# Performance work log

Hardware: AMD Instinct MI355X
Metric: run time of the kernel (lower is better)

## Reference

```python
import jax, jax.numpy as jnp
import numpy as np

EPS = 1e-5
NB, NP, NA, NROT = 16, 1024, 12, 60
C0, C1 = 64, 128
CIN, CFEAT, COUT = 256, 512, 256


def _bn(x, g, b):
    # training-mode BatchNorm1d: stats over batch (+ spatial) dims, channel dim 1
    axes = (0,) if x.ndim == 2 else (0, 2)
    m = x.mean(axis=axes, keepdims=True)
    v = x.var(axis=axes, keepdims=True)
    sh = [1] * x.ndim; sh[1] = -1
    return (x - m) * jax.lax.rsqrt(v + EPS) * g.reshape(sh) + b.reshape(sh)


def _hat(v):  # (n,3) -> (n,3,3) skew-symmetric
    z = jnp.zeros_like(v[:, 0])
    return jnp.stack([z, -v[:, 2], v[:, 1],
                      v[:, 2], z, -v[:, 0],
                      -v[:, 1], v[:, 0], z], axis=-1).reshape(-1, 3, 3)


def _exp_so3(v):  # Rodrigues formula, (n,3) -> (n,3,3)
    theta = jnp.linalg.norm(v, axis=-1, keepdims=True)  # (n,1)
    k = v / jnp.where(theta < 1e-8, 1.0, theta)
    K = _hat(k)
    s = jnp.sin(theta)[..., None]
    c = (1.0 - jnp.cos(theta))[..., None]
    I = jnp.eye(3, dtype=v.dtype)
    return I + s * K + c * (K @ K)


def _pointnet(xyz, feats, W, b, g, bb):
    # PointnetSO3Conv: concat xyz (expanded over anchors) with feats, 1x1 conv, max over points
    nb, _, npts, na = feats.shape
    x = jnp.concatenate([jnp.broadcast_to(xyz[:, :, :, None], (nb, 3, npts, na)), feats], axis=1)
    y = jnp.einsum('oc,bcpa->bopa', W, x) + b[None, :, None, None]
    y = y.max(axis=2)  # max over points -> (nb, o, na)
    return jax.nn.relu(_bn(y, g, bb))


def setup_inputs() -> dict:
    key = jax.random.key(0)
    ks = iter(jax.random.split(key, 64))
    def nrm(shape, s=0.1):
        return jax.random.normal(next(ks), shape, dtype=jnp.float32) * s
    d = {
        'xyz0': nrm((NB, 3, NP), 1.0),
        'feats0': nrm((NB, C0, NP, NA), 1.0),
        'xyz1': nrm((NB, 3, NP), 1.0),
        'feats1': nrm((NB, C1, NP, NA), 1.0),
        'trace_idx': jax.random.randint(next(ks), (NA, NROT), 0, NA),
        'anchors': nrm((NROT, 3, 3), 1.0),
        'pn0_W': nrm((C0, C0 + 3)), 'pn0_b': nrm((C0,)), 'pn0_g': jnp.ones((C0,), jnp.float32), 'pn0_bb': jnp.zeros((C0,), jnp.float32),
        'pn1_W': nrm((C1, C1 + 3)), 'pn1_b': nrm((C1,)), 'pn1_g': jnp.ones((C1,), jnp.float32), 'pn1_bb': jnp.zeros((C1,), jnp.float32),
        'lin_W': nrm((CIN, C0 + C1)), 'lin_b': nrm((CIN,)), 'lin_g': jnp.ones((CIN,), jnp.float32), 'lin_bb': jnp.zeros((CIN,), jnp.float32),
        'feat_W': nrm((CFEAT, CIN * NA)), 'feat_b': nrm((CFEAT,)), 'feat_g': jnp.ones((CFEAT,), jnp.float32), 'feat_bb': jnp.zeros((CFEAT,), jnp.float32),
        'att_W1': nrm((128, CFEAT)), 'att_b1': nrm((128,)), 'att_g': jnp.ones((128,), jnp.float32), 'att_bb': jnp.zeros((128,), jnp.float32),
        'att_W2': nrm((1, 128)), 'att_b2': nrm((1,)),
        'reg_W1': nrm((128, CFEAT)), 'reg_b1': nrm((128,)), 'reg_g': jnp.ones((128,), jnp.float32), 'reg_bb': jnp.zeros((128,), jnp.float32),
        'reg_W2': nrm((7, 128)), 'reg_b2': nrm((7,)),
        'out_W1': nrm((CFEAT, CFEAT)), 'out_b1': nrm((CFEAT,)), 'out_g': jnp.ones((CFEAT,), jnp.float32), 'out_bb': jnp.zeros((CFEAT,), jnp.float32),
        'out_W2': nrm((COUT, CFEAT)), 'out_b2': nrm((COUT,)),
    }
    return d


def reference(xyz0, feats0, xyz1, feats1, trace_idx, anchors,
              pn0_W, pn0_b, pn0_g, pn0_bb, pn1_W, pn1_b, pn1_g, pn1_bb,
              lin_W, lin_b, lin_g, lin_bb, feat_W, feat_b, feat_g, feat_bb,
              att_W1, att_b1, att_g, att_bb, att_W2, att_b2,
              reg_W1, reg_b1, reg_g, reg_bb, reg_W2, reg_b2,
              out_W1, out_b1, out_g, out_bb, out_W2, out_b2):
    nb = feats0.shape[0]
    # _pooling: per-level pointnet + BN + relu, concat, pn_linear + pn_bn
    p0 = _pointnet(xyz0, feats0, pn0_W, pn0_b, pn0_g, pn0_bb)
    p1 = _pointnet(xyz1, feats1, pn1_W, pn1_b, pn1_g, pn1_bb)
    x = jnp.concatenate([p0, p1], axis=1)                                   # (nb, 192, na)
    x = _bn(jnp.einsum('oc,bca->boa', lin_W, x) + lin_b[None, :, None], lin_g, lin_bb)  # (nb,256,na)
    # gather trace_idx_ori and flatten channel x anchor dims
    x = x[:, :, trace_idx].reshape(nb, CIN * NA, NROT)                      # (nb,3072,60)
    xf = jax.nn.relu(_bn(jnp.einsum('oc,bca->boa', feat_W, x) + feat_b[None, :, None], feat_g, feat_bb))  # (nb,512,60)
    h = jax.nn.relu(_bn(jnp.einsum('oc,bca->boa', reg_W1, xf) + reg_b1[None, :, None], reg_g, reg_bb))
    residual = (jnp.einsum('oc,bca->boa', reg_W2, h) + reg_b2[None, :, None]).transpose(0, 2, 1)  # (nb,60,7)
    res_D = residual[:, :, :3] / jnp.linalg.norm(residual[:, :, :3], axis=-1, keepdims=True)
    res_N = (jax.nn.sigmoid(residual[:, :, 3]) - 0.5) * jnp.pi / 5
    res_V = res_D * res_N[..., None]
    res_R = _exp_so3(res_V.reshape(-1, 3)).reshape(nb, NROT, 3, 3)
    res_T = residual[:, :, 4:]
    pred_R = jnp.einsum('tij,btjk->btik', anchors, res_R)
    # attention head + softmax over 60 rotations
    a = jax.nn.relu(_bn(jnp.einsum('oc,bca->boa', att_W1, xf) + att_b1[None, :, None], att_g, att_bb))
    logits = (jnp.einsum('oc,bca->boa', att_W2, a) + att_b2[None, :, None])[:, 0]   # (nb,60)
    x_attn = jax.nn.softmax(logits, axis=-1)
    # max-pool over rotations + out MLP
    xm = xf.max(axis=-1)                                                    # (nb,512)
    o = jax.nn.relu(_bn(xm @ out_W1.T + out_b1, out_g, out_bb))
    x_out = o @ out_W2.T + out_b2
    return (x_out, x_attn, pred_R, res_T)
```

## Files before the change

### kernel.cpp

```cpp
#include <hip/hip_runtime.h>
#include <math.h>

#define NBATCH 16
#define NPTS   1024
#define NANG   12
#define NROTS  60
#define EPSV   1e-5f

#define WB0_OFF   0
#define WB1_OFF   3072
#define PART0_OFF 13312
#define PART1_OFF 799744
#define FEATW_OFF 13312
#define XF_OFF    13312
#define XM_OFF    504832
#define OACT_OFF  513024
#define XCAT_OFF  2372608
#define XLIN_OFF  2409472
#define XG_OFF    2458624
#define BRP_OFF   2458624
#define HACT_OFF  4424704
#define AACT_OFF  4547584
#define FRAW_OFF  5604352

#define OUT_XOUT 0
#define OUT_ATTN 4096
#define OUT_PRED 5056
#define OUT_REST 13696

typedef short  bf16x8 __attribute__((ext_vector_type(8)));
typedef float  f32x4  __attribute__((ext_vector_type(4)));

__device__ __forceinline__ unsigned short f2bf_rne(float x){
  unsigned int u = __float_as_uint(x);
  u += 0x7FFFu + ((u >> 16) & 1u);
  return (unsigned short)(u >> 16);
}
__device__ __forceinline__ float bf2f(unsigned short h){
  return __uint_as_float(((unsigned int)h) << 16);
}

__device__ __forceinline__ bf16x8 pack8(const float* f){
  union { unsigned int u[4]; bf16x8 v; } r;
  #pragma unroll
  for (int i = 0; i < 4; i++)
    r.u[i] = __builtin_amdgcn_perm(__float_as_uint(f[2*i+1]),
                                   __float_as_uint(f[2*i]), 0x07060302u);
  return r.v;
}

template<int NT>
__device__ __forceinline__ void block_stats(float v, float& m, float& var, float* sbuf){
  constexpr int NW = NT / 64;
  float s = v, s2 = v * v;
  #pragma unroll
  for (int off = 32; off; off >>= 1){
    s  += __shfl_xor(s,  off, 64);
    s2 += __shfl_xor(s2, off, 64);
  }
  const int w = threadIdx.x >> 6;
  if ((threadIdx.x & 63) == 0){ sbuf[w] = s; sbuf[NW + w] = s2; }
  __syncthreads();
  float ts = 0.f, ts2 = 0.f;
  #pragma unroll
  for (int i = 0; i < NW; i++){ ts += sbuf[i]; ts2 += sbuf[NW + i]; }
  m = ts / (float)NT;
  var = ts2 / (float)NT - m * m;
}

template<int C>
__global__ void prep_wb(const float* __restrict__ W, unsigned short* __restrict__ Wb){
  constexpr int KPAD = C + 32;
  const int idx = blockIdx.x * 256 + threadIdx.x;
  if (idx >= C * KPAD) return;
  const int o = idx / KPAD, k = idx % KPAD;
  float v = 0.f;
  if (k < C)          v = W[(size_t)o * (C + 3) + 3 + k];
  else if (k < C + 3) v = W[(size_t)o * (C + 3) + (k - C)];
  Wb[idx] = f2bf_rne(v);
}

template<int C>
__global__ __launch_bounds__(256) void pn_mfma(
    const float* __restrict__ xyz, const float* __restrict__ feats,
    const unsigned short* __restrict__ Wb, float* __restrict__ part){
  constexpr int KPAD = C + 32;
  constexpr int NK   = KPAD / 32;
  constexpr int MT   = C / 16;
  const int nchunk = blockIdx.x, b = blockIdx.y;
  const int tid  = threadIdx.x;
  const int lane = tid & 63, wave = tid >> 6;
  const int g = lane >> 4, l16 = lane & 15;
  const int colbase = wave * 48;
  const int nbase   = nchunk * 192;

  int nn[3], pp[3];
  #pragma unroll
  for (int t = 0; t < 3; t++){
    nn[t] = nbase + colbase + t * 16 + l16;
    pp[t] = nn[t] / 12;
  }

  f32x4 acc[MT][3];
  #pragma unroll
  for (int m = 0; m < MT; m++)
    #pragma unroll
    for (int t = 0; t < 3; t++)
      acc[m][t] = (f32x4){0.f, 0.f, 0.f, 0.f};

  const float* fB = feats + (size_t)b * C * (NPTS * NANG);

  #pragma unroll
  for (int ks = 0; ks < NK - 1; ks++){
    const int kb = ks * 32;
    bf16x8 Bf[3];
    #pragma unroll
    for (int t = 0; t < 3; t++){
      const float* src = fB + (size_t)(kb + g * 8) * (NPTS * NANG) + nn[t];
      float f[8];
      #pragma unroll
      for (int j = 0; j < 8; j++) f[j] = src[(size_t)j * (NPTS * NANG)];
      Bf[t] = pack8(f);
    }
    #pragma unroll
    for (int m = 0; m < MT; m++){
      const bf16x8 Af = *(const bf16x8*)(Wb + (size_t)(m * 16 + l16) * KPAD + kb + g * 8);
      #pragma unroll
      for (int t = 0; t < 3; t++)
        acc[m][t] = __builtin_amdgcn_mfma_f32_16x16x32_bf16(Af, Bf[t], acc[m][t], 0, 0, 0);
    }
  }

  {
    const int kb = C;
    bf16x8 Bf[3];
    #pragma unroll
    for (int t = 0; t < 3; t++){
      float f[8];
      #pragma unroll
      for (int j = 0; j < 8; j++) f[j] = 0.f;
      if (g == 0){
        #pragma unroll
        for (int j = 0; j < 3; j++)
          f[j] = xyz[(size_t)(b * 3 + j) * NPTS + pp[t]];
      }
      Bf[t] = pack8(f);
    }
    #pragma unroll
    for (int m = 0; m < MT; m++){
      const bf16x8 Af = *(const bf16x8*)(Wb + (size_t)(m * 16 + l16) * KPAD + kb + g * 8);
      #pragma unroll
      for (int t = 0; t < 3; t++)
        acc[m][t] = __builtin_amdgcn_mfma_f32_16x16x32_bf16(Af, Bf[t], acc[m][t], 0, 0, 0);
    }
  }

  __shared__ float yb[16 * 192];
  #pragma unroll
  for (int m = 0; m < MT; m++){
    __syncthreads();
    #pragma unroll
    for (int t = 0; t < 3; t++)
      #pragma unroll
      for (int r = 0; r < 4; r++)
        yb[(g * 4 + r) * 192 + colbase + t * 16 + l16] = acc[m][t][r];
    __syncthreads();
    if (tid < 192){
      const int o_l = tid / 12, a = tid % 12;
      float mx = -3.4e38f;
      #pragma unroll
      for (int pl = 0; pl < 16; pl++)
        mx = fmaxf(mx, yb[o_l * 192 + pl * 12 + a]);
      part[(((size_t)b * C + m * 16 + o_l) * 12 + a) * 64 + nchunk] = mx;
    }
  }
}

__global__ void pn_reduce_bn(const float* __restrict__ part0, const float* __restrict__ part1,
    const float* __restrict__ b0, const float* __restrict__ g0, const float* __restrict__ bb0,
    const float* __restrict__ b1, const float* __restrict__ g1, const float* __restrict__ bb1,
    float* __restrict__ xcat){
  const int ch = blockIdx.x, t = threadIdx.x;
  const int b = t / 12, a = t % 12;
  const float* part; const float *bias, *g, *bb; int o, Cl;
  if (ch < 64){ part = part0; bias = b0; g = g0; bb = bb0; o = ch;      Cl = 64;  }
  else        { part = part1; bias = b1; g = g1; bb = bb1; o = ch - 64; Cl = 128; }
  const float* pp = part + (((size_t)b * Cl + o) * 12 + a) * 64;
  float v = pp[0];
  for (int k = 1; k < 64; k++) v = fmaxf(v, pp[k]);
  v += bias[o];
  __shared__ float sbuf[8];
  float m, var;
  block_stats<192>(v, m, var, sbuf);
  float xn = (v - m) * rsqrtf(var + EPSV) * g[o] + bb[o];
  xcat[((size_t)b * 192 + ch) * 12 + a] = fmaxf(xn, 0.f);
}

__global__ void lin_bn(const float* __restrict__ xcat, const float* __restrict__ W,
    const float* __restrict__ bias, const float* __restrict__ g, const float* __restrict__ bb,
    float* __restrict__ xlin){
  const int o = blockIdx.x, t = threadIdx.x;
  const int b = t / 12, a = t % 12;
  const float* xr = xcat + (size_t)b * 2304 + a;
  const float* wr = W + (size_t)o * 192;
  float v = bias[o];
  for (int c = 0; c < 192; c++) v = fmaf(wr[c], xr[(size_t)c * 12], v);
  __shared__ float sbuf[8];
  float m, var;
  block_stats<192>(v, m, var, sbuf);
  xlin[((size_t)b * 256 + o) * 12 + a] = (v - m) * rsqrtf(var + EPSV) * g[o] + bb[o];
}

__global__ void prep_featw(const float* __restrict__ W, unsigned short* __restrict__ Wb2){
  const int idx = blockIdx.x * 256 + threadIdx.x;
  if (idx >= 512 * 3072) return;
  const int o = idx / 3072, k = idx % 3072;
  const float x = W[idx];
  const unsigned short hi = f2bf_rne(x);
  const unsigned short lo = f2bf_rne(x - bf2f(hi));
  Wb2[(size_t)o * 6144 + k] = hi;
  Wb2[(size_t)o * 6144 + 3072 + k] = lo;
}

__global__ void prep_xg(const float* __restrict__ xlin, const int* __restrict__ trace,
                        unsigned short* __restrict__ Xg){
  const int n = blockIdx.x;
  const int r = n & 63, b = n >> 6;
  unsigned short* row = Xg + (size_t)n * 6144;
  if (r >= 60){
    for (int i = threadIdx.x; i < 3072; i += 256){ row[i] = 0; row[3072 + i] = 0; }
    return;
  }
  __shared__ int ta[12];
  if (threadIdx.x < 12) ta[threadIdx.x] = trace[threadIdx.x * 60 + r];
  __syncthreads();
  for (int i = threadIdx.x; i < 3072; i += 256){
    const int c = i / 12, a = i % 12;
    const float x = xlin[((size_t)b * 256 + c) * 12 + ta[a]];
    const unsigned short hi = f2bf_rne(x);
    const unsigned short lo = f2bf_rne(x - bf2f(hi));
    row[i] = hi;
    row[3072 + i] = lo;
  }
}

__global__ __launch_bounds__(256) void feat_mfma(
    const unsigned short* __restrict__ Wb2, const unsigned short* __restrict__ Xg,
    float* __restrict__ fraw){
  const int b = blockIdx.x, mblk = blockIdx.y, job = blockIdx.z;
  const int lane = threadIdx.x & 63, wave = threadIdx.x >> 6;
  const int g = lane >> 4, l16 = lane & 15;
  const int wm = (wave >> 1) * 2;
  const int wn = (wave & 1) * 2;
  const int koff  = (job & 1) * 1536;
  const int npass = (job >> 1) + 1;

  const size_t rowA0 = (size_t)(mblk * 64 + (wm + 0) * 16 + l16) * 6144;
  const size_t rowA1 = (size_t)(mblk * 64 + (wm + 1) * 16 + l16) * 6144;
  const size_t rowB0 = (size_t)(b * 64 + (wn + 0) * 16 + l16) * 6144;
  const size_t rowB1 = (size_t)(b * 64 + (wn + 1) * 16 + l16) * 6144;

  f32x4 acc00 = {0.f,0.f,0.f,0.f}, acc01 = {0.f,0.f,0.f,0.f};
  f32x4 acc10 = {0.f,0.f,0.f,0.f}, acc11 = {0.f,0.f,0.f,0.f};

  for (int p = 0; p < npass; p++){
    int kA = 0, kB = 0;
    if (npass == 2){ if (p == 0) kA = 3072; else kB = 3072; }
    const unsigned short* A0p = Wb2 + rowA0 + kA + koff + g * 8;
    const unsigned short* A1p = Wb2 + rowA1 + kA + koff + g * 8;
    const unsigned short* B0p = Xg  + rowB0 + kB + koff + g * 8;
    const unsigned short* B1p = Xg  + rowB1 + kB + koff + g * 8;

    bf16x8 a0 = *(const bf16x8*)A0p, a1 = *(const bf16x8*)A1p;
    bf16x8 b0 = *(const bf16x8*)B0p, b1 = *(const bf16x8*)B1p;

    #pragma unroll 4
    for (int kb = 32; kb < 1536; kb += 32){
      const bf16x8 na0 = *(const bf16x8*)(A0p + kb);
      const bf16x8 na1 = *(const bf16x8*)(A1p + kb);
      const bf16x8 nb0 = *(const bf16x8*)(B0p + kb);
      const bf16x8 nb1 = *(const bf16x8*)(B1p + kb);
      acc00 = __builtin_amdgcn_mfma_f32_16x16x32_bf16(a0, b0, acc00, 0, 0, 0);
      acc01 = __builtin_amdgcn_mfma_f32_16x16x32_bf16(a0, b1, acc01, 0, 0, 0);
      acc10 = __builtin_amdgcn_mfma_f32_16x16x32_bf16(a1, b0, acc10, 0, 0, 0);
      acc11 = __builtin_amdgcn_mfma_f32_16x16x32_bf16(a1, b1, acc11, 0, 0, 0);
      a0 = na0; a1 = na1; b0 = nb0; b1 = nb1;
    }
    acc00 = __builtin_amdgcn_mfma_f32_16x16x32_bf16(a0, b0, acc00, 0, 0, 0);
    acc01 = __builtin_amdgcn_mfma_f32_16x16x32_bf16(a0, b1, acc01, 0, 0, 0);
    acc10 = __builtin_amdgcn_mfma_f32_16x16x32_bf16(a1, b0, acc10, 0, 0, 0);
    acc11 = __builtin_amdgcn_mfma_f32_16x16x32_bf16(a1, b1, acc11, 0, 0, 0);
  }

  float* base = fraw + ((size_t)job * NBATCH + b) * (512 * 60);
  const int r0 = (wn + 0) * 16 + l16;
  const int r1 = (wn + 1) * 16 + l16;
  #pragma unroll
  for (int q = 0; q < 4; q++){
    const int o0 = mblk * 64 + (wm + 0) * 16 + g * 4 + q;
    const int o1 = mblk * 64 + (wm + 1) * 16 + g * 4 + q;
    if (r0 < 60){
      base[(size_t)o0 * 60 + r0] = acc00[q];
      base[(size_t)o1 * 60 + r0] = acc10[q];
    }
    if (r1 < 60){
      base[(size_t)o0 * 60 + r1] = acc01[q];
      base[(size_t)o1 * 60 + r1] = acc11[q];
    }
  }
}

__global__ void feat_bn(const float* __restrict__ fraw, const float* __restrict__ bias,
    const float* __restrict__ g, const float* __restrict__ bb,
    float* __restrict__ xf, float* __restrict__ xm){
  const int o = blockIdx.x, t = threadIdx.x;
  const int b = t / 60, r = t % 60;
  const size_t i0 = ((size_t)b * 512 + o) * 60 + r;
  const size_t SS = (size_t)NBATCH * 512 * 60;
  float v = fraw[i0] + fraw[SS + i0] + fraw[2 * SS + i0] + fraw[3 * SS + i0] + bias[o];
  __shared__ float sbuf[32];
  float m, var;
  block_stats<960>(v, m, var, sbuf);
  const float xn = fmaxf((v - m) * rsqrtf(var + EPSV) * g[o] + bb[o], 0.f);
  xf[i0] = xn;
  __shared__ float red[960];
  red[t] = xn;
  __syncthreads();
  if (r == 0){
    float mx = red[t];
    for (int k = 1; k < 60; k++) mx = fmaxf(mx, red[t + k]);
    xm[(size_t)b * 512 + o] = mx;
  }
}

__global__ __launch_bounds__(256) void brgemm2(const float* __restrict__ xf,
    const float* __restrict__ Wr, const float* __restrict__ Wa,
    float* __restrict__ brp){
  const int og = blockIdx.x, b = blockIdx.y, z = blockIdx.z;
  const int br = z >> 3, ks = z & 7;
  const float* W = br ? Wa : Wr;
  const int lane = threadIdx.x & 63, wave = threadIdx.x >> 6;
  const int obase = og * 32 + wave * 8;
  const int rr = lane < 60 ? lane : 0;
  const float* xb = xf + ((size_t)b * 512 + ks * 64) * 60 + rr;
  const float* wr = W + (size_t)obase * 512 + ks * 64;

  float acc[8];
  #pragma unroll
  for (int i = 0; i < 8; i++) acc[i] = 0.f;

  float cur[4], nxt[4];
  #pragma unroll
  for (int j = 0; j < 4; j++) cur[j] = xb[(size_t)j * 60];

  for (int c0 = 0; c0 < 64; c0 += 4){
    #pragma unroll
    for (int j = 0; j < 4; j++){
      int cc = c0 + 4 + j; if (cc > 63) cc = 63;
      nxt[j] = xb[(size_t)cc * 60];
    }
    #pragma unroll
    for (int j = 0; j < 4; j++)
      #pragma unroll
      for (int i = 0; i < 8; i++)
        acc[i] = fmaf(wr[(size_t)i * 512 + c0 + j], cur[j], acc[i]);
    #pragma unroll
    for (int j = 0; j < 4; j++) cur[j] = nxt[j];
  }

  if (lane < 60){
    #pragma unroll
    for (int i = 0; i < 8; i++)
      brp[(((size_t)z * NBATCH + b) * 128 + obase + i) * 60 + lane] = acc[i];
  }
}

__global__ void br_bn(const float* __restrict__ brp,
    const float* __restrict__ biasR, const float* __restrict__ gR, const float* __restrict__ bbR,
    const float* __restrict__ biasA, const float* __restrict__ gA, const float* __restrict__ bbA,
    float* __restrict__ hact, float* __restrict__ aact){
  const int o = blockIdx.x, br = blockIdx.y, t = threadIdx.x;
  const int b = t / 60, r = t % 60;
  const float* bias = br ? biasA : biasR;
  const float* g    = br ? gA    : gR;
  const float* bb   = br ? bbA   : bbR;
  float v = bias[o];
  #pragma unroll
  for (int ks = 0; ks < 8; ks++)
    v += brp[((((size_t)br * 8 + ks) * NBATCH + b) * 128 + o) * 60 + r];
  __shared__ float sbuf[32];
  float m, var;
  block_stats<960>(v, m, var, sbuf);
  float* outp = br ? aact : hact;
  outp[((size_t)b * 128 + o) * 60 + r] =
      fmaxf((v - m) * rsqrtf(var + EPSV) * g[o] + bb[o], 0.f);
}

__global__ void reg2_geom(const float* __restrict__ h, const float* __restrict__ W2,
    const float* __restrict__ b2, const float* __restrict__ anchors, float* __restrict__ out){
  const int b = blockIdx.x, lane = threadIdx.x;
  const int r = lane < 60 ? lane : 59;
  float res[7];
  #pragma unroll
  for (int j = 0; j < 7; j++){
    float acc = b2[j];
    for (int c = 0; c < 128; c++)
      acc = fmaf(W2[j * 128 + c], h[((size_t)b * 128 + c) * 60 + r], acc);
    res[j] = acc;
  }
  if (lane >= 60) return;
  const float n = sqrtf(res[0]*res[0] + res[1]*res[1] + res[2]*res[2]);
  const float invn = 1.f / n;
  const float Nv = (1.f / (1.f + expf(-res[3])) - 0.5f) * 3.14159265358979323846f / 5.f;
  const float v0 = res[0]*invn*Nv, v1 = res[1]*invn*Nv, v2 = res[2]*invn*Nv;
  const float th = sqrtf(v0*v0 + v1*v1 + v2*v2);
  const float invt = th < 1e-8f ? 1.f : 1.f / th;
  const float k0 = v0*invt, k1 = v1*invt, k2 = v2*invt;
  const float s = sinf(th), cc = 1.f - cosf(th);
  const float K[9] = {0.f, -k2, k1,  k2, 0.f, -k0,  -k1, k0, 0.f};
  float K2[9];
  #pragma unroll
  for (int ii = 0; ii < 3; ii++)
    #pragma unroll
    for (int jj = 0; jj < 3; jj++)
      K2[ii*3+jj] = K[ii*3+0]*K[0*3+jj] + K[ii*3+1]*K[1*3+jj] + K[ii*3+2]*K[2*3+jj];
  float R[9];
  #pragma unroll
  for (int ii = 0; ii < 3; ii++)
    #pragma unroll
    for (int jj = 0; jj < 3; jj++)
      R[ii*3+jj] = (ii == jj ? 1.f : 0.f) + s * K[ii*3+jj] + cc * K2[ii*3+jj];
  const float* A = anchors + (size_t)r * 9;
  #pragma unroll
  for (int ii = 0; ii < 3; ii++)
    #pragma unroll
    for (int kk = 0; kk < 3; kk++){
      const float pv = A[ii*3+0]*R[0*3+kk] + A[ii*3+1]*R[1*3+kk] + A[ii*3+2]*R[2*3+kk];
      out[OUT_PRED + ((size_t)b * 60 + r) * 9 + ii * 3 + kk] = pv;
    }
  #pragma unroll
  for (int k = 0; k < 3; k++)
    out[OUT_REST + ((size_t)b * 60 + r) * 3 + k] = res[4 + k];
}

__global__ void att2_softmax(const float* __restrict__ a, const float* __restrict__ W2,
    const float* __restrict__ b2, float* __restrict__ out){
  const int b = blockIdx.x, lane = threadIdx.x;
  const int r = lane < 60 ? lane : 59;
  float acc = b2[0];
  for (int c = 0; c < 128; c++)
    acc = fmaf(W2[c], a[((size_t)b * 128 + c) * 60 + r], acc);
  const float l = lane < 60 ? acc : -INFINITY;
  float mx = l;
  #pragma unroll
  for (int off = 32; off; off >>= 1) mx = fmaxf(mx, __shfl_xor(mx, off, 64));
  const float e = lane < 60 ? expf(l - mx) : 0.f;
  float ssum = e;
  #pragma unroll
  for (int off = 32; off; off >>= 1) ssum += __shfl_xor(ssum, off, 64);
  if (lane < 60) out[OUT_ATTN + (size_t)b * 60 + lane] = e / ssum;
}

__global__ void out_head1(const float* __restrict__ xm, const float* __restrict__ W1,
    const float* __restrict__ b1, const float* __restrict__ g, const float* __restrict__ bb,
    float* __restrict__ o_act){
  const int t = threadIdx.x;
  const int b = t & 15, j = t >> 4;
  const int oc = blockIdx.x * 8 + j;
  float acc = b1[oc];
  const float* wr = W1 + (size_t)oc * 512;
  const float* xr = xm + (size_t)b * 512;
  for (int c = 0; c < 512; c++) acc = fmaf(wr[c], xr[c], acc);
  float s = acc, s2 = acc * acc;
  #pragma unroll
  for (int off = 8; off; off >>= 1){
    s  += __shfl_xor(s,  off, 16);
    s2 += __shfl_xor(s2, off, 16);
  }
  const float m = s * (1.f / 16.f);
  const float var = s2 * (1.f / 16.f) - m * m;
  o_act[(size_t)b * 512 + oc] = fmaxf((acc - m) * rsqrtf(var + EPSV) * g[oc] + bb[oc], 0.f);
}

__global__ void out_head2(const float* __restrict__ o_act, const float* __restrict__ W2,
    const float* __restrict__ b2, float* __restrict__ out){
  const int b = blockIdx.x, j = threadIdx.x;
  const float* wr = W2 + (size_t)j * 512;
  const float* xr = o_act + (size_t)b * 512;
  float acc = b2[j];
  for (int c = 0; c < 512; c++) acc = fmaf(wr[c], xr[c], acc);
  out[OUT_XOUT + (size_t)b * 256 + j] = acc;
}

extern "C" void kernel_launch(void* const* d_in, const int* in_sizes, int n_in,
                              void* d_out, int out_size, void* d_ws, size_t ws_size,
                              hipStream_t stream){
  const float* xyz0    = (const float*)d_in[0];
  const float* feats0  = (const float*)d_in[1];
  const float* xyz1    = (const float*)d_in[2];
  const float* feats1  = (const float*)d_in[3];
  const int*   trace   = (const int*)  d_in[4];
  const float* anchors = (const float*)d_in[5];
  const float* pn0_W  = (const float*)d_in[6];
  const float* pn0_b  = (const float*)d_in[7];
  const float* pn0_g  = (const float*)d_in[8];
  const float* pn0_bb = (const float*)d_in[9];
  const float* pn1_W  = (const float*)d_in[10];
  const float* pn1_b  = (const float*)d_in[11];
  const float* pn1_g  = (const float*)d_in[12];
  const float* pn1_bb = (const float*)d_in[13];
  const float* lin_W  = (const float*)d_in[14];
  const float* lin_b  = (const float*)d_in[15];
  const float* lin_g  = (const float*)d_in[16];
  const float* lin_bb = (const float*)d_in[17];
  const float* feat_W  = (const float*)d_in[18];
  const float* feat_b  = (const float*)d_in[19];
  const float* feat_g  = (const float*)d_in[20];
  const float* feat_bb = (const float*)d_in[21];
  const float* att_W1 = (const float*)d_in[22];
  const float* att_b1 = (const float*)d_in[23];
  const float* att_g  = (const float*)d_in[24];
  const float* att_bb = (const float*)d_in[25];
  const float* att_W2 = (const float*)d_in[26];
  const float* att_b2 = (const float*)d_in[27];
  const float* reg_W1 = (const float*)d_in[28];
  const float* reg_b1 = (const float*)d_in[29];
  const float* reg_g  = (const float*)d_in[30];
  const float* reg_bb = (const float*)d_in[31];
  const float* reg_W2 = (const float*)d_in[32];
  const float* reg_b2 = (const float*)d_in[33];
  const float* out_W1 = (const float*)d_in[34];
  const float* out_b1 = (const float*)d_in[35];
  const float* out_g  = (const float*)d_in[36];
  const float* out_bb = (const float*)d_in[37];
  const float* out_W2 = (const float*)d_in[38];
  const float* out_b2 = (const float*)d_in[39];

  float* ws  = (float*)d_ws;
  float* out = (float*)d_out;
  unsigned short* wb0 = (unsigned short*)(ws + WB0_OFF);
  unsigned short* wb1 = (unsigned short*)(ws + WB1_OFF);
  unsigned short* fw  = (unsigned short*)(ws + FEATW_OFF);
  unsigned short* xg  = (unsigned short*)(ws + XG_OFF);

  prep_wb<64> <<<24, 256, 0, stream>>>(pn0_W, wb0);
  prep_wb<128><<<80, 256, 0, stream>>>(pn1_W, wb1);

  pn_mfma<64> <<<dim3(64, 16), 256, 0, stream>>>(xyz0, feats0, wb0, ws + PART0_OFF);
  pn_mfma<128><<<dim3(64, 16), 256, 0, stream>>>(xyz1, feats1, wb1, ws + PART1_OFF);

  pn_reduce_bn<<<192, 192, 0, stream>>>(ws + PART0_OFF, ws + PART1_OFF,
      pn0_b, pn0_g, pn0_bb, pn1_b, pn1_g, pn1_bb, ws + XCAT_OFF);

  prep_featw<<<6144, 256, 0, stream>>>(feat_W, fw);

  lin_bn<<<256, 192, 0, stream>>>(ws + XCAT_OFF, lin_W, lin_b, lin_g, lin_bb, ws + XLIN_OFF);

  prep_xg<<<1024, 256, 0, stream>>>(ws + XLIN_OFF, trace, xg);

  feat_mfma<<<dim3(16, 8, 4), 256, 0, stream>>>(fw, xg, ws + FRAW_OFF);
  feat_bn<<<512, 960, 0, stream>>>(ws + FRAW_OFF, feat_b, feat_g, feat_bb,
                                   ws + XF_OFF, ws + XM_OFF);

  brgemm2<<<dim3(4, 16, 16), 256, 0, stream>>>(ws + XF_OFF, reg_W1, att_W1, ws + BRP_OFF);
  br_bn<<<dim3(128, 2), 960, 0, stream>>>(ws + BRP_OFF,
      reg_b1, reg_g, reg_bb, att_b1, att_g, att_bb,
      ws + HACT_OFF, ws + AACT_OFF);

  reg2_geom<<<16, 64, 0, stream>>>(ws + HACT_OFF, reg_W2, reg_b2, anchors, out);
  att2_softmax<<<16, 64, 0, stream>>>(ws + AACT_OFF, att_W2, att_b2, out);
  out_head1<<<64, 128, 0, stream>>>(ws + XM_OFF, out_W1, out_b1, out_g, out_bb, ws + OACT_OFF);
  out_head2<<<16, 256, 0, stream>>>(ws + OACT_OFF, out_W2, out_b2, out);
}
```

Before: 521.0 us.

## Stage feat GEMM tiles through LDS with async global-to-LDS loads and pack rows

The feature GEMM now stages 64x64 bf16 tiles of weights and gathered inputs into double-buffered LDS using global_load_lds with an XOR swizzle. Previously each wave read its operands directly from global memory. Rows are packed densely (960 instead of 16x64 with padding), so the zero-padded rows and their wasted MFMA work go away. The split-bf16 passes go from four K-split jobs to three full-K segments, which feat_bn reduces with fewer partials. The aims are better operand reuse and less wasted compute, at the cost of LDS use and a barrier per K chunk.

```diff
diff --git a/kernel.cpp b/kernel.cpp
--- a/kernel.cpp
+++ b/kernel.cpp
@@ -21,7 +21,7 @@
 #define BRP_OFF   2458624
 #define HACT_OFF  4424704
 #define AACT_OFF  4547584
-#define FRAW_OFF  5604352
+#define FRAW_OFF  5407744
 
 #define OUT_XOUT 0
 #define OUT_ATTN 4096
@@ -47,6 +47,11 @@
     r.u[i] = __builtin_amdgcn_perm(__float_as_uint(f[2*i+1]),
                                    __float_as_uint(f[2*i]), 0x07060302u);
   return r.v;
+}
+
+__device__ __forceinline__ void stage16(const unsigned short* g, unsigned short* l){
+  __builtin_amdgcn_global_load_lds((const __attribute__((address_space(1))) void*)g,
+                                   (__attribute__((address_space(3))) void*)l, 16, 0, 0);
 }
 
 template<int NT>
@@ -225,12 +230,8 @@
 __global__ void prep_xg(const float* __restrict__ xlin, const int* __restrict__ trace,
                         unsigned short* __restrict__ Xg){
   const int n = blockIdx.x;
-  const int r = n & 63, b = n >> 6;
+  const int b = n / 60, r = n % 60;
   unsigned short* row = Xg + (size_t)n * 6144;
-  if (r >= 60){
-    for (int i = threadIdx.x; i < 3072; i += 256){ row[i] = 0; row[3072 + i] = 0; }
-    return;
-  }
   __shared__ int ta[12];
   if (threadIdx.x < 12) ta[threadIdx.x] = trace[threadIdx.x * 60 + r];
   __syncthreads();
@@ -247,67 +248,84 @@
 __global__ __launch_bounds__(256) void feat_mfma(
     const unsigned short* __restrict__ Wb2, const unsigned short* __restrict__ Xg,
     float* __restrict__ fraw){
-  const int b = blockIdx.x, mblk = blockIdx.y, job = blockIdx.z;
-  const int lane = threadIdx.x & 63, wave = threadIdx.x >> 6;
+  const int nblk = blockIdx.x, mblk = blockIdx.y, seg = blockIdx.z;
+  const int tid = threadIdx.x;
+  const int lane = tid & 63, wave = tid >> 6;
   const int g = lane >> 4, l16 = lane & 15;
-  const int wm = (wave >> 1) * 2;
-  const int wn = (wave & 1) * 2;
-  const int koff  = (job & 1) * 1536;
-  const int npass = (job >> 1) + 1;
-
-  const size_t rowA0 = (size_t)(mblk * 64 + (wm + 0) * 16 + l16) * 6144;
-  const size_t rowA1 = (size_t)(mblk * 64 + (wm + 1) * 16 + l16) * 6144;
-  const size_t rowB0 = (size_t)(b * 64 + (wn + 0) * 16 + l16) * 6144;
-  const size_t rowB1 = (size_t)(b * 64 + (wn + 1) * 16 + l16) * 6144;
-
-  f32x4 acc00 = {0.f,0.f,0.f,0.f}, acc01 = {0.f,0.f,0.f,0.f};
-  f32x4 acc10 = {0.f,0.f,0.f,0.f}, acc11 = {0.f,0.f,0.f,0.f};
-
-  for (int p = 0; p < npass; p++){
-    int kA = 0, kB = 0;
-    if (npass == 2){ if (p == 0) kA = 3072; else kB = 3072; }
-    const unsigned short* A0p = Wb2 + rowA0 + kA + koff + g * 8;
-    const unsigned short* A1p = Wb2 + rowA1 + kA + koff + g * 8;
-    const unsigned short* B0p = Xg  + rowB0 + kB + koff + g * 8;
-    const unsigned short* B1p = Xg  + rowB1 + kB + koff + g * 8;
-
-    bf16x8 a0 = *(const bf16x8*)A0p, a1 = *(const bf16x8*)A1p;
-    bf16x8 b0 = *(const bf16x8*)B0p, b1 = *(const bf16x8*)B1p;
-
-    #pragma unroll 4
-    for (int kb = 32; kb < 1536; kb += 32){
-      const bf16x8 na0 = *(const bf16x8*)(A0p + kb);
-      const bf16x8 na1 = *(const bf16x8*)(A1p + kb);
-      const bf16x8 nb0 = *(const bf16x8*)(B0p + kb);
-      const bf16x8 nb1 = *(const bf16x8*)(B1p + kb);
-      acc00 = __builtin_amdgcn_mfma_f32_16x16x32_bf16(a0, b0, acc00, 0, 0, 0);
-      acc01 = __builtin_amdgcn_mfma_f32_16x16x32_bf16(a0, b1, acc01, 0, 0, 0);
-      acc10 = __builtin_amdgcn_mfma_f32_16x16x32_bf16(a1, b0, acc10, 0, 0, 0);
-      acc11 = __builtin_amdgcn_mfma_f32_16x16x32_bf16(a1, b1, acc11, 0, 0, 0);
-      a0 = na0; a1 = na1; b0 = nb0; b1 = nb1;
-    }
-    acc00 = __builtin_amdgcn_mfma_f32_16x16x32_bf16(a0, b0, acc00, 0, 0, 0);
-    acc01 = __builtin_amdgcn_mfma_f32_16x16x32_bf16(a0, b1, acc01, 0, 0, 0);
-    acc10 = __builtin_amdgcn_mfma_f32_16x16x32_bf16(a1, b0, acc10, 0, 0, 0);
-    acc11 = __builtin_amdgcn_mfma_f32_16x16x32_bf16(a1, b1, acc11, 0, 0, 0);
-  }
-
-  float* base = fraw + ((size_t)job * NBATCH + b) * (512 * 60);
-  const int r0 = (wn + 0) * 16 + l16;
-  const int r1 = (wn + 1) * 16 + l16;
-  #pragma unroll
-  for (int q = 0; q < 4; q++){
-    const int o0 = mblk * 64 + (wm + 0) * 16 + g * 4 + q;
-    const int o1 = mblk * 64 + (wm + 1) * 16 + g * 4 + q;
-    if (r0 < 60){
-      base[(size_t)o0 * 60 + r0] = acc00[q];
-      base[(size_t)o1 * 60 + r0] = acc10[q];
-    }
-    if (r1 < 60){
-      base[(size_t)o0 * 60 + r1] = acc01[q];
-      base[(size_t)o1 * 60 + r1] = acc11[q];
-    }
-  }
+  const int kA = (seg == 1) ? 3072 : 0;
+  const int kB = (seg == 2) ? 3072 : 0;
+  const int sw = l16 & 7;
+  const int wm = wave >> 1, wn = wave & 1;
+
+  __shared__ unsigned short As[2][64 * 64];
+  __shared__ unsigned short Bs[2][64 * 64];
+
+  int rowj[2], colj[2], ldsoff[2];
+  #pragma unroll
+  for (int j = 0; j < 2; j++){
+    const int idx = j * 256 + wave * 64 + lane;
+    rowj[j]   = idx >> 3;
+    colj[j]   = ((idx & 7) ^ (rowj[j] & 7)) * 8;
+    ldsoff[j] = (j * 256 + wave * 64) * 8;
+  }
+  const unsigned short* Agb = Wb2 + (size_t)mblk * 64 * 6144 + kA;
+  const unsigned short* Bgb = Xg  + (size_t)nblk * 64 * 6144 + kB;
+
+  f32x4 acc[2][2];
+  #pragma unroll
+  for (int i = 0; i < 2; i++)
+    #pragma unroll
+    for (int j = 0; j < 2; j++)
+      acc[i][j] = (f32x4){0.f, 0.f, 0.f, 0.f};
+
+  #pragma unroll
+  for (int j = 0; j < 2; j++){
+    stage16(Agb + (size_t)rowj[j] * 6144 + colj[j], &As[0][ldsoff[j]]);
+    stage16(Bgb + (size_t)rowj[j] * 6144 + colj[j], &Bs[0][ldsoff[j]]);
+  }
+  __syncthreads();
+
+  for (int kc = 0; kc < 3072; kc += 64){
+    const int buf = (kc >> 6) & 1;
+    if (kc + 64 < 3072){
+      const int kn = kc + 64;
+      #pragma unroll
+      for (int j = 0; j < 2; j++){
+        stage16(Agb + (size_t)rowj[j] * 6144 + kn + colj[j], &As[buf ^ 1][ldsoff[j]]);
+        stage16(Bgb + (size_t)rowj[j] * 6144 + kn + colj[j], &Bs[buf ^ 1][ldsoff[j]]);
+      }
+    }
+    #pragma unroll
+    for (int kc2 = 0; kc2 < 64; kc2 += 32){
+      const int c0 = kc2 >> 3;
+      bf16x8 af[2], bfr[2];
+      #pragma unroll
+      for (int i = 0; i < 2; i++)
+        af[i]  = *(const bf16x8*)&As[buf][(wm * 32 + i * 16 + l16) * 64 + ((c0 + g) ^ sw) * 8];
+      #pragma unroll
+      for (int i = 0; i < 2; i++)
+        bfr[i] = *(const bf16x8*)&Bs[buf][(wn * 32 + i * 16 + l16) * 64 + ((c0 + g) ^ sw) * 8];
+      #pragma unroll
+      for (int i = 0; i < 2; i++)
+        #pragma unroll
+        for (int j = 0; j < 2; j++)
+          acc[i][j] = __builtin_amdgcn_mfma_f32_16x16x32_bf16(af[i], bfr[j], acc[i][j], 0, 0, 0);
+    }
+    __syncthreads();
+  }
+
+  float* base = fraw + (size_t)seg * (512 * 960);
+  #pragma unroll
+  for (int i = 0; i < 2; i++)
+    #pragma unroll
+    for (int j = 0; j < 2; j++){
+      const int n = nblk * 64 + wn * 32 + j * 16 + l16;
+      #pragma unroll
+      for (int q = 0; q < 4; q++){
+        const int m = mblk * 64 + wm * 32 + i * 16 + g * 4 + q;
+        base[(size_t)m * 960 + n] = acc[i][j][q];
+      }
+    }
 }
 
 __global__ void feat_bn(const float* __restrict__ fraw, const float* __restrict__ bias,
@@ -315,14 +333,14 @@
     float* __restrict__ xf, float* __restrict__ xm){
   const int o = blockIdx.x, t = threadIdx.x;
   const int b = t / 60, r = t % 60;
-  const size_t i0 = ((size_t)b * 512 + o) * 60 + r;
-  const size_t SS = (size_t)NBATCH * 512 * 60;
-  float v = fraw[i0] + fraw[SS + i0] + fraw[2 * SS + i0] + fraw[3 * SS + i0] + bias[o];
+  const size_t SS = (size_t)512 * 960;
+  const size_t in = (size_t)o * 960 + t;
+  float v = fraw[in] + fraw[SS + in] + fraw[2 * SS + in] + bias[o];
   __shared__ float sbuf[32];
   float m, var;
   block_stats<960>(v, m, var, sbuf);
   const float xn = fmaxf((v - m) * rsqrtf(var + EPSV) * g[o] + bb[o], 0.f);
-  xf[i0] = xn;
+  xf[((size_t)b * 512 + o) * 60 + r] = xn;
   __shared__ float red[960];
   red[t] = xn;
   __syncthreads();
@@ -556,9 +574,9 @@
 
   lin_bn<<<256, 192, 0, stream>>>(ws + XCAT_OFF, lin_W, lin_b, lin_g, lin_bb, ws + XLIN_OFF);
 
-  prep_xg<<<1024, 256, 0, stream>>>(ws + XLIN_OFF, trace, xg);
-
-  feat_mfma<<<dim3(16, 8, 4), 256, 0, stream>>>(fw, xg, ws + FRAW_OFF);
+  prep_xg<<<960, 256, 0, stream>>>(ws + XLIN_OFF, trace, xg);
+
+  feat_mfma<<<dim3(15, 8, 3), 256, 0, stream>>>(fw, xg, ws + FRAW_OFF);
   feat_bn<<<512, 960, 0, stream>>>(ws + FRAW_OFF, feat_b, feat_g, feat_bb,
                                    ws + XF_OFF, ws + XM_OFF);
 
```

Result: faster. 496.7 us (-4.7%).
